# Kernel tuning notes

Hardware: AMD Instinct MI355X
Metric: run time of the kernel (lower is better)

Reference implementation:

```python
import jax, jax.numpy as jnp
import numpy as np

SCALE = 0.1  # literal .mul(0.1) in the source, not 1/sqrt(d_k)


def setup_inputs() -> dict:
    key = jax.random.key(0)
    kq, kk, kv = jax.random.split(key, 3)
    B, S, D, Dv = 8, 2048, 1024, 1024
    q = jax.random.normal(kq, (B, S, D), dtype=jnp.float32)
    k = jax.random.normal(kk, (B, D, S), dtype=jnp.float32)  # note [B, D, S]: matmul(q, k) with no transpose
    v = jax.random.normal(kv, (B, S, Dv), dtype=jnp.float32)
    return {"q": q, "k": k, "v": v}


def reference(q, k, v):
    # s = (q @ k) * 0.1 ; a = softmax(s, -1) ; dropout in eval -> identity ; r = a @ v
    s = jnp.einsum('bsd,bdt->bst', q, k) * SCALE  # [B, S, S]
    a = jax.nn.softmax(s, axis=-1)
    r = jnp.einsum('bst,btv->bsv', a, v)          # [B, S, Dv]
    return r
```

## Files before the change

kernel.cpp:

```cpp
#include <hip/hip_runtime.h>
#include <stdint.h>

#define SEQ 2048
#define DHK 1024
#define DHV 1024
#define NB 8

typedef __attribute__((ext_vector_type(8))) short bf16x8;
typedef __attribute__((ext_vector_type(4))) float f32x4;

__device__ __forceinline__ unsigned short f2bf(float f) {
    uint32_t u = __builtin_bit_cast(uint32_t, f);
    u += 0x7fffu + ((u >> 16) & 1u);
    return (unsigned short)(u >> 16);
}

__device__ __forceinline__ void gload_lds16(const unsigned short* g, unsigned short* l) {
    __builtin_amdgcn_global_load_lds(
        (const __attribute__((address_space(1))) void*)g,
        (__attribute__((address_space(3))) void*)l,
        16, 0, 0);
}

__global__ __launch_bounds__(256) void cvt_q(const float* __restrict__ in,
                                             unsigned short* __restrict__ out) {
    size_t i = ((size_t)blockIdx.x * 256 + threadIdx.x) * 8;
    float4 v0 = *(const float4*)(in + i);
    float4 v1 = *(const float4*)(in + i + 4);
    ushort4 o0, o1;
    o0.x = f2bf(v0.x); o0.y = f2bf(v0.y); o0.z = f2bf(v0.z); o0.w = f2bf(v0.w);
    o1.x = f2bf(v1.x); o1.y = f2bf(v1.y); o1.z = f2bf(v1.z); o1.w = f2bf(v1.w);
    *(ushort4*)(out + i) = o0;
    *(ushort4*)(out + i + 4) = o1;
}

__global__ __launch_bounds__(256) void tr_cvt(const float* __restrict__ in,
                                              unsigned short* __restrict__ out,
                                              int R, int C) {
    __shared__ unsigned short tile[64][72];
    int b  = blockIdx.z;
    int c0 = blockIdx.x * 64, r0 = blockIdx.y * 64;
    const float* ib = in + (size_t)b * R * C;
    unsigned short* ob = out + (size_t)b * R * C;
    int tr = threadIdx.x >> 4;
    int tc = (threadIdx.x & 15) * 4;
#pragma unroll
    for (int it = 0; it < 4; ++it) {
        int r = tr + it * 16;
        float4 v = *(const float4*)(ib + (size_t)(r0 + r) * C + c0 + tc);
        tile[r][tc + 0] = f2bf(v.x);
        tile[r][tc + 1] = f2bf(v.y);
        tile[r][tc + 2] = f2bf(v.z);
        tile[r][tc + 3] = f2bf(v.w);
    }
    __syncthreads();
#pragma unroll
    for (int it = 0; it < 4; ++it) {
        int r = tr + it * 16;
        ushort4 o;
        o.x = tile[tc + 0][r];
        o.y = tile[tc + 1][r];
        o.z = tile[tc + 2][r];
        o.w = tile[tc + 3][r];
        *(ushort4*)(ob + (size_t)(c0 + r) * R + r0 + tc) = o;
    }
}

template <int MODE>
__global__ __launch_bounds__(256) void attn_gemm(const unsigned short* __restrict__ A,
                                                 const unsigned short* __restrict__ Bt,
                                                 int K, int N,
                                                 void* __restrict__ Cout,
                                                 float* __restrict__ L) {
    __shared__ unsigned short As[128 * 32];
    __shared__ unsigned short Bs[128 * 32];
    const int tid  = threadIdx.x;
    const int w    = tid >> 6;
    const int lane = tid & 63;
    const int wm   = w & 1, wn = w >> 1;
    const int b  = blockIdx.z;
    const int bm = blockIdx.y, bn = blockIdx.x;
    const unsigned short* Ab = A + (size_t)b * SEQ * K;
    const unsigned short* Bb = Bt + (size_t)b * N * K;

    const int lr = lane >> 2, ls = lane & 3;
    size_t goffA[2], goffB[2];
#pragma unroll
    for (int c = 0; c < 2; ++c) {
        int rloc = w * 32 + c * 16 + lr;
        int g    = ls ^ ((rloc >> 1) & 3);
        goffA[c] = (size_t)(bm * 128 + rloc) * K + g * 8;
        goffB[c] = (size_t)(bn * 128 + rloc) * K + g * 8;
    }
    unsigned short* ldsA0 = &As[(w * 32 + 0) * 32];
    unsigned short* ldsA1 = &As[(w * 32 + 16) * 32];
    unsigned short* ldsB0 = &Bs[(w * 32 + 0) * 32];
    unsigned short* ldsB1 = &Bs[(w * 32 + 16) * 32];

    f32x4 acc[4][4];
#pragma unroll
    for (int i = 0; i < 4; ++i)
#pragma unroll
        for (int j = 0; j < 4; ++j)
#pragma unroll
            for (int e = 0; e < 4; ++e) acc[i][j][e] = 0.0f;

    const int m16 = lane & 15, q = lane >> 4;

    for (int kk = 0; kk < K; kk += 32) {
        gload_lds16(Ab + goffA[0] + kk, ldsA0);
        gload_lds16(Ab + goffA[1] + kk, ldsA1);
        gload_lds16(Bb + goffB[0] + kk, ldsB0);
        gload_lds16(Bb + goffB[1] + kk, ldsB1);
        __syncthreads();
        bf16x8 af[4], bfv[4];
#pragma unroll
        for (int t = 0; t < 4; ++t) {
            int rl = wm * 64 + t * 16 + m16;
            af[t]  = *(const bf16x8*)&As[rl * 32 + (q ^ ((rl >> 1) & 3)) * 8];
            int rb = wn * 64 + t * 16 + m16;
            bfv[t] = *(const bf16x8*)&Bs[rb * 32 + (q ^ ((rb >> 1) & 3)) * 8];
        }
#pragma unroll
        for (int mt = 0; mt < 4; ++mt)
#pragma unroll
            for (int nt = 0; nt < 4; ++nt)
                acc[mt][nt] = __builtin_amdgcn_mfma_f32_16x16x32_bf16(af[mt], bfv[nt],
                                                                      acc[mt][nt], 0, 0, 0);
        __syncthreads();
    }

    const int i0 = bm * 128 + wm * 64;
    const int t0 = bn * 128 + wn * 64;
    if (MODE == 0) {
        unsigned short* E = (unsigned short*)Cout + (size_t)b * SEQ * N;
        float rs[4][4];
#pragma unroll
        for (int mt = 0; mt < 4; ++mt)
#pragma unroll
            for (int e = 0; e < 4; ++e) rs[mt][e] = 0.0f;
#pragma unroll
        for (int mt = 0; mt < 4; ++mt)
#pragma unroll
            for (int nt = 0; nt < 4; ++nt)
#pragma unroll
                for (int e = 0; e < 4; ++e) {
                    float v = __expf(0.1f * acc[mt][nt][e]);
                    int i = i0 + mt * 16 + q * 4 + e;
                    int t = t0 + nt * 16 + m16;
                    E[(size_t)i * N + t] = f2bf(v);
                    rs[mt][e] += v;
                }
#pragma unroll
        for (int mt = 0; mt < 4; ++mt)
#pragma unroll
            for (int e = 0; e < 4; ++e) {
                float v = rs[mt][e];
                v += __shfl_xor(v, 1);
                v += __shfl_xor(v, 2);
                v += __shfl_xor(v, 4);
                v += __shfl_xor(v, 8);
                if (m16 == 0) atomicAdd(&L[b * SEQ + i0 + mt * 16 + q * 4 + e], v);
            }
    } else {
        float* O = (float*)Cout + (size_t)b * SEQ * N;
#pragma unroll
        for (int mt = 0; mt < 4; ++mt)
#pragma unroll
            for (int e = 0; e < 4; ++e) {
                int i = i0 + mt * 16 + q * 4 + e;
                float inv = 1.0f / L[b * SEQ + i];
#pragma unroll
                for (int nt = 0; nt < 4; ++nt) {
                    int t = t0 + nt * 16 + m16;
                    O[(size_t)i * N + t] = acc[mt][nt][e] * inv;
                }
            }
    }
}

extern "C" void kernel_launch(void* const* d_in, const int* in_sizes, int n_in,
                              void* d_out, int out_size, void* d_ws, size_t ws_size,
                              hipStream_t stream) {
    (void)in_sizes; (void)n_in; (void)out_size; (void)ws_size;
    const float* q = (const float*)d_in[0];
    const float* k = (const float*)d_in[1];
    const float* v = (const float*)d_in[2];

    char* ws = (char*)d_ws;
    unsigned short* Qb = (unsigned short*)(ws);
    unsigned short* Kt = (unsigned short*)(ws + 33554432);
    unsigned short* Vt = (unsigned short*)(ws + 67108864);
    unsigned short* E  = (unsigned short*)(ws + 100663296);
    float* L           = (float*)(ws + 167772160);

    hipMemsetAsync(L, 0, NB * SEQ * sizeof(float), stream);

    cvt_q<<<dim3((NB * SEQ * DHK) / (256 * 8)), dim3(256), 0, stream>>>(q, Qb);
    tr_cvt<<<dim3(SEQ / 64, DHK / 64, NB), dim3(256), 0, stream>>>(k, Kt, DHK, SEQ);
    tr_cvt<<<dim3(DHV / 64, SEQ / 64, NB), dim3(256), 0, stream>>>(v, Vt, SEQ, DHV);

    attn_gemm<0><<<dim3(SEQ / 128, SEQ / 128, NB), dim3(256), 0, stream>>>(Qb, Kt, DHK, SEQ,
                                                                           (void*)E, L);
    attn_gemm<1><<<dim3(DHV / 128, SEQ / 128, NB), dim3(256), 0, stream>>>(E, Vt, SEQ, DHV,
                                                                           d_out, L);
}
```

Baseline: 438.6 us.

## Double K-step per barrier, remap blocks for L2 locality, fp32 transpose tile

The GEMM kernels now stage 64-wide K slices in LDS with an 8-way XOR swizzle, which halves the number of barrier pairs per tile. They also use a 1D grid with batch-interleaved, panel-grouped block remapping so neighbouring blocks share A and B tiles in L2. K and N become compile-time constants. The transpose kernel stores fp32 in a padded tile and converts on the way out, which changes the LDS bank pattern. Together these aim to cut sync overhead and DRAM traffic, at the cost of more LDS per block.

```diff
diff --git a/kernel.cpp b/kernel.cpp
--- a/kernel.cpp
+++ b/kernel.cpp
@@ -37,7 +37,7 @@
 __global__ __launch_bounds__(256) void tr_cvt(const float* __restrict__ in,
                                               unsigned short* __restrict__ out,
                                               int R, int C) {
-    __shared__ unsigned short tile[64][72];
+    __shared__ float tile[64][65];
     int b  = blockIdx.z;
     int c0 = blockIdx.x * 64, r0 = blockIdx.y * 64;
     const float* ib = in + (size_t)b * R * C;
@@ -48,54 +48,67 @@
     for (int it = 0; it < 4; ++it) {
         int r = tr + it * 16;
         float4 v = *(const float4*)(ib + (size_t)(r0 + r) * C + c0 + tc);
-        tile[r][tc + 0] = f2bf(v.x);
-        tile[r][tc + 1] = f2bf(v.y);
-        tile[r][tc + 2] = f2bf(v.z);
-        tile[r][tc + 3] = f2bf(v.w);
+        tile[r][tc + 0] = v.x; tile[r][tc + 1] = v.y;
+        tile[r][tc + 2] = v.z; tile[r][tc + 3] = v.w;
     }
     __syncthreads();
 #pragma unroll
     for (int it = 0; it < 4; ++it) {
-        int r = tr + it * 16;
+        int c = tr + it * 16;
         ushort4 o;
-        o.x = tile[tc + 0][r];
-        o.y = tile[tc + 1][r];
-        o.z = tile[tc + 2][r];
-        o.w = tile[tc + 3][r];
-        *(ushort4*)(ob + (size_t)(c0 + r) * R + r0 + tc) = o;
+        o.x = f2bf(tile[tc + 0][c]);
+        o.y = f2bf(tile[tc + 1][c]);
+        o.z = f2bf(tile[tc + 2][c]);
+        o.w = f2bf(tile[tc + 3][c]);
+        *(ushort4*)(ob + (size_t)(c0 + c) * R + r0 + tc) = o;
     }
 }
 
 template <int MODE>
 __global__ __launch_bounds__(256) void attn_gemm(const unsigned short* __restrict__ A,
                                                  const unsigned short* __restrict__ Bt,
-                                                 int K, int N,
                                                  void* __restrict__ Cout,
                                                  float* __restrict__ L) {
-    __shared__ unsigned short As[128 * 32];
-    __shared__ unsigned short Bs[128 * 32];
+    constexpr int K  = (MODE == 0) ? DHK : SEQ;
+    constexpr int N  = (MODE == 0) ? SEQ : DHV;
+    constexpr int GM = SEQ / 128;
+    constexpr int GN = N / 128;
+    constexpr int PM = (MODE == 0) ? 8 : 4;
+    constexpr int PN = (MODE == 0) ? 8 : 4;
+    constexpr int NPM = GM / PM;
+
+    __shared__ unsigned short As[128 * 64];
+    __shared__ unsigned short Bs[128 * 64];
+
+    int lid   = blockIdx.x;
+    int batch = lid & 7;
+    int t     = lid >> 3;
+    int pi    = t / (PM * PN);
+    int wio   = t % (PM * PN);
+    int bm    = (pi % NPM) * PM + (wio % PM);
+    int bn    = (pi / NPM) * PN + (wio / PM);
+
     const int tid  = threadIdx.x;
-    const int w    = tid >> 6;
+    const int wv   = tid >> 6;
     const int lane = tid & 63;
-    const int wm   = w & 1, wn = w >> 1;
-    const int b  = blockIdx.z;
-    const int bm = blockIdx.y, bn = blockIdx.x;
-    const unsigned short* Ab = A + (size_t)b * SEQ * K;
-    const unsigned short* Bb = Bt + (size_t)b * N * K;
-
-    const int lr = lane >> 2, ls = lane & 3;
-    size_t goffA[2], goffB[2];
-#pragma unroll
-    for (int c = 0; c < 2; ++c) {
-        int rloc = w * 32 + c * 16 + lr;
-        int g    = ls ^ ((rloc >> 1) & 3);
-        goffA[c] = (size_t)(bm * 128 + rloc) * K + g * 8;
-        goffB[c] = (size_t)(bn * 128 + rloc) * K + g * 8;
-    }
-    unsigned short* ldsA0 = &As[(w * 32 + 0) * 32];
-    unsigned short* ldsA1 = &As[(w * 32 + 16) * 32];
-    unsigned short* ldsB0 = &Bs[(w * 32 + 0) * 32];
-    unsigned short* ldsB1 = &Bs[(w * 32 + 16) * 32];
+    const int wm   = wv & 1, wn = wv >> 1;
+    const int m16  = lane & 15, q = lane >> 4;
+
+    const unsigned short* Ab = A + (size_t)batch * SEQ * K;
+    const unsigned short* Bb = Bt + (size_t)batch * N * K;
+
+    const int lr8 = lane >> 3;
+    const int g   = (lane & 7) ^ lr8;
+    size_t gA[4], gB[4];
+    unsigned short *lA[4], *lB[4];
+#pragma unroll
+    for (int c = 0; c < 4; ++c) {
+        int rloc = wv * 32 + c * 8 + lr8;
+        gA[c] = (size_t)(bm * 128 + rloc) * K + g * 8;
+        gB[c] = (size_t)(bn * 128 + rloc) * K + g * 8;
+        lA[c] = &As[(wv * 32 + c * 8) * 64];
+        lB[c] = &Bs[(wv * 32 + c * 8) * 64];
+    }
 
     f32x4 acc[4][4];
 #pragma unroll
@@ -105,35 +118,38 @@
 #pragma unroll
             for (int e = 0; e < 4; ++e) acc[i][j][e] = 0.0f;
 
-    const int m16 = lane & 15, q = lane >> 4;
-
-    for (int kk = 0; kk < K; kk += 32) {
-        gload_lds16(Ab + goffA[0] + kk, ldsA0);
-        gload_lds16(Ab + goffA[1] + kk, ldsA1);
-        gload_lds16(Bb + goffB[0] + kk, ldsB0);
-        gload_lds16(Bb + goffB[1] + kk, ldsB1);
+    const int sw = m16 & 7;
+
+    for (int kk = 0; kk < K; kk += 64) {
+#pragma unroll
+        for (int c = 0; c < 4; ++c) gload_lds16(Ab + gA[c] + kk, lA[c]);
+#pragma unroll
+        for (int c = 0; c < 4; ++c) gload_lds16(Bb + gB[c] + kk, lB[c]);
         __syncthreads();
-        bf16x8 af[4], bfv[4];
-#pragma unroll
-        for (int t = 0; t < 4; ++t) {
-            int rl = wm * 64 + t * 16 + m16;
-            af[t]  = *(const bf16x8*)&As[rl * 32 + (q ^ ((rl >> 1) & 3)) * 8];
-            int rb = wn * 64 + t * 16 + m16;
-            bfv[t] = *(const bf16x8*)&Bs[rb * 32 + (q ^ ((rb >> 1) & 3)) * 8];
+#pragma unroll
+        for (int ss = 0; ss < 2; ++ss) {
+            bf16x8 af[4], bfv[4];
+#pragma unroll
+            for (int tt = 0; tt < 4; ++tt) {
+                int rl = wm * 64 + tt * 16 + m16;
+                af[tt]  = *(const bf16x8*)&As[rl * 64 + ((ss * 4 + q) ^ sw) * 8];
+                int rb = wn * 64 + tt * 16 + m16;
+                bfv[tt] = *(const bf16x8*)&Bs[rb * 64 + ((ss * 4 + q) ^ sw) * 8];
+            }
+#pragma unroll
+            for (int mt = 0; mt < 4; ++mt)
+#pragma unroll
+                for (int nt = 0; nt < 4; ++nt)
+                    acc[mt][nt] = __builtin_amdgcn_mfma_f32_16x16x32_bf16(
+                        af[mt], bfv[nt], acc[mt][nt], 0, 0, 0);
         }
-#pragma unroll
-        for (int mt = 0; mt < 4; ++mt)
-#pragma unroll
-            for (int nt = 0; nt < 4; ++nt)
-                acc[mt][nt] = __builtin_amdgcn_mfma_f32_16x16x32_bf16(af[mt], bfv[nt],
-                                                                      acc[mt][nt], 0, 0, 0);
         __syncthreads();
     }
 
     const int i0 = bm * 128 + wm * 64;
     const int t0 = bn * 128 + wn * 64;
     if (MODE == 0) {
-        unsigned short* E = (unsigned short*)Cout + (size_t)b * SEQ * N;
+        unsigned short* E = (unsigned short*)Cout + (size_t)batch * SEQ * N;
         float rs[4][4];
 #pragma unroll
         for (int mt = 0; mt < 4; ++mt)
@@ -147,8 +163,8 @@
                 for (int e = 0; e < 4; ++e) {
                     float v = __expf(0.1f * acc[mt][nt][e]);
                     int i = i0 + mt * 16 + q * 4 + e;
-                    int t = t0 + nt * 16 + m16;
-                    E[(size_t)i * N + t] = f2bf(v);
+                    int tt = t0 + nt * 16 + m16;
+                    E[(size_t)i * N + tt] = f2bf(v);
                     rs[mt][e] += v;
                 }
 #pragma unroll
@@ -160,20 +176,20 @@
                 v += __shfl_xor(v, 2);
                 v += __shfl_xor(v, 4);
                 v += __shfl_xor(v, 8);
-                if (m16 == 0) atomicAdd(&L[b * SEQ + i0 + mt * 16 + q * 4 + e], v);
+                if (m16 == 0) atomicAdd(&L[batch * SEQ + i0 + mt * 16 + q * 4 + e], v);
             }
     } else {
-        float* O = (float*)Cout + (size_t)b * SEQ * N;
+        float* O = (float*)Cout + (size_t)batch * SEQ * N;
 #pragma unroll
         for (int mt = 0; mt < 4; ++mt)
 #pragma unroll
             for (int e = 0; e < 4; ++e) {
                 int i = i0 + mt * 16 + q * 4 + e;
-                float inv = 1.0f / L[b * SEQ + i];
+                float inv = 1.0f / L[batch * SEQ + i];
 #pragma unroll
                 for (int nt = 0; nt < 4; ++nt) {
-                    int t = t0 + nt * 16 + m16;
-                    O[(size_t)i * N + t] = acc[mt][nt][e] * inv;
+                    int tt = t0 + nt * 16 + m16;
+                    O[(size_t)i * N + tt] = acc[mt][nt][e] * inv;
                 }
             }
     }
@@ -200,8 +216,6 @@
     tr_cvt<<<dim3(SEQ / 64, DHK / 64, NB), dim3(256), 0, stream>>>(k, Kt, DHK, SEQ);
     tr_cvt<<<dim3(DHV / 64, SEQ / 64, NB), dim3(256), 0, stream>>>(v, Vt, SEQ, DHV);
 
-    attn_gemm<0><<<dim3(SEQ / 128, SEQ / 128, NB), dim3(256), 0, stream>>>(Qb, Kt, DHK, SEQ,
-                                                                           (void*)E, L);
-    attn_gemm<1><<<dim3(DHV / 128, SEQ / 128, NB), dim3(256), 0, stream>>>(E, Vt, SEQ, DHV,
-                                                                           d_out, L);
-}
+    attn_gemm<0><<<dim3(NB * 16 * 16), dim3(256), 0, stream>>>(Qb, Kt, (void*)E, L);
+    attn_gemm<1><<<dim3(NB * 16 * 8), dim3(256), 0, stream>>>(E, Vt, d_out, L);
+}
```

New measurement: 407.6 us. 1.08x faster.
